# Performance work log

Hardware: AMD Instinct MI355X
Metric: run time of the kernel (lower is better)

Reference implementation:

```python
import jax, jax.numpy as jnp
import numpy as np

N_CHANNELS = 512
N_HEAD = 8
N_GROUPS = 32
EPS = 1e-5


def setup_inputs() -> dict:
    key = jax.random.key(0)
    ks = jax.random.split(key, 12)
    C = N_CHANNELS
    s = 1.0 / np.sqrt(C)
    return {
        "x": jax.random.normal(ks[0], (16, C, 32, 32), dtype=jnp.float32),
        "gn_w": jnp.ones((C,), jnp.float32),
        "gn_b": jnp.zeros((C,), jnp.float32),
        "conv_w": jax.random.normal(ks[1], (C, C), dtype=jnp.float32) * s,  # 1x1 conv kernel [out,in]
        "conv_b": jnp.zeros((C,), jnp.float32),
        "wq": jax.random.normal(ks[2], (C, C), dtype=jnp.float32) * s,  # torch Linear weight [out,in]
        "bq": jnp.zeros((C,), jnp.float32),
        "wk": jax.random.normal(ks[3], (C, C), dtype=jnp.float32) * s,
        "bk": jnp.zeros((C,), jnp.float32),
        "wv": jax.random.normal(ks[4], (C, C), dtype=jnp.float32) * s,
        "bv": jnp.zeros((C,), jnp.float32),
        "wo": jax.random.normal(ks[5], (C, C), dtype=jnp.float32) * s,
        "bo": jnp.zeros((C,), jnp.float32),
    }


def _group_norm(x, w, b):
    # x: [B, C, H, W]; normalize over channel groups + spatial dims
    B, C, H, W = x.shape
    xg = x.reshape(B, N_GROUPS, C // N_GROUPS, H, W)
    mean = jnp.mean(xg, axis=(2, 3, 4), keepdims=True)
    var = jnp.var(xg, axis=(2, 3, 4), keepdims=True)
    xn = ((xg - mean) * jax.lax.rsqrt(var + EPS)).reshape(B, C, H, W)
    return xn * w[None, :, None, None] + b[None, :, None, None]


def reference(x, gn_w, gn_b, conv_w, conv_b, wq, bq, wk, bk, wv, bv, wo, bo):
    B, C, H, W = x.shape
    nh, dk = N_HEAD, C // N_HEAD
    scale = dk ** -0.5

    xn = _group_norm(x, gn_w, gn_b)
    # 1x1 conv == per-pixel linear over channels
    x1 = jnp.einsum("bchw,oc->bohw", xn, conv_w) + conv_b[None, :, None, None]
    # b c h w -> b (h w) c
    x1 = x1.reshape(B, C, H * W).transpose(0, 2, 1)  # [B, L, C]

    q = x1 @ wq.T + bq
    k = x1 @ wk.T + bk
    v = x1 @ wv.T + bv

    L = H * W
    # b l (n d) -> b n l d
    q = q.reshape(B, L, nh, dk).transpose(0, 2, 1, 3)
    k = k.reshape(B, L, nh, dk).transpose(0, 2, 1, 3)
    v = v.reshape(B, L, nh, dk).transpose(0, 2, 1, 3)

    attn = jnp.einsum("bnid,bnjd->bnij", q, k) * scale
    score = jax.nn.softmax(attn, axis=-1)
    res = jnp.einsum("bnij,bnjd->bnid", score, v)

    # b n l d -> b l (n d)
    res = res.transpose(0, 2, 1, 3).reshape(B, L, C)
    res = res @ wo.T + bo
    # b l c -> b c h w
    res = res.transpose(0, 2, 1).reshape(B, C, H, W)
    return res + x
```

## Files before the change

### kernel.cpp

```cpp
#include <hip/hip_runtime.h>
#include <math.h>

typedef __attribute__((ext_vector_type(4))) float f4;
typedef __attribute__((ext_vector_type(16))) float f16v;
typedef __attribute__((ext_vector_type(8))) short s8;
typedef __attribute__((ext_vector_type(4))) unsigned short u16x4;
typedef unsigned short u16;
typedef unsigned int u32;

constexpr int kB = 16, kC = 512, kL = 1024, kNH = 8, kG = 32;
constexpr float kEps = 1e-5f;
constexpr float kQScale = 0.18033688011112042f;

__device__ __forceinline__ u16 f2bf(float f) {
    union { float f; unsigned u; } c; c.f = f;
    unsigned u = c.u;
    return (u16)((u + 0x7fffu + ((u >> 16) & 1u)) >> 16);
}
__device__ __forceinline__ float bf2f(u16 v) {
    union { u32 u; float f; } c; c.u = (u32)v << 16; return c.f;
}
__device__ __forceinline__ u32 pkbf(float lo, float hi) {
    u32 r;
    asm("v_cvt_pk_bf16_f32 %0, %1, %2" : "=v"(r) : "v"(lo), "v"(hi));
    return r;
}

__device__ __forceinline__ void gload_lds16(const void* g, void* l) {
    __builtin_amdgcn_global_load_lds(
        (const __attribute__((address_space(1))) void*)g,
        (__attribute__((address_space(3))) void*)l, 16, 0, 0);
}

__global__ __launch_bounds__(256)
void gn_stats_kernel(const float* __restrict__ x, float2* __restrict__ stats)
{
    const int bg = blockIdx.x;
    const float4* p = (const float4*)(x + (size_t)bg * (16 * kL));
    float s = 0.f, ss = 0.f;
    for (int i = threadIdx.x; i < (16 * kL) / 4; i += 256) {
        float4 v = p[i];
        s  += v.x + v.y + v.z + v.w;
        ss += v.x * v.x + v.y * v.y + v.z * v.z + v.w * v.w;
    }
    #pragma unroll
    for (int off = 32; off > 0; off >>= 1) {
        s  += __shfl_down(s, off);
        ss += __shfl_down(ss, off);
    }
    __shared__ float rs[4], rss[4];
    if ((threadIdx.x & 63) == 0) { rs[threadIdx.x >> 6] = s; rss[threadIdx.x >> 6] = ss; }
    __syncthreads();
    if (threadIdx.x == 0) {
        float S = rs[0] + rs[1] + rs[2] + rs[3];
        float SS = rss[0] + rss[1] + rss[2] + rss[3];
        const float inv_n = 1.f / (float)(16 * kL);
        float mean = S * inv_n;
        float var  = SS * inv_n - mean * mean;
        stats[bg] = make_float2(mean, rsqrtf(var + kEps));
    }
}

__global__ __launch_bounds__(256)
void wprep_kernel(const float* __restrict__ wq, const float* __restrict__ wk,
                  const float* __restrict__ wv, const float* __restrict__ wo,
                  const float* __restrict__ cw,
                  u16* __restrict__ dst, u16* __restrict__ dstT)
{
    __shared__ float t[64][65];
    const int tid = threadIdx.x;
    if (blockIdx.x < 1024) {
        int idx = blockIdx.x * 256 + tid;
        int m = idx >> 16;
        int r = idx & 65535;
        const float* srcs[4] = {wq, wk, wv, wo};
        float4 v = ((const float4*)srcs[m])[r];
        u16x4 o; o.x = f2bf(v.x); o.y = f2bf(v.y); o.z = f2bf(v.z); o.w = f2bf(v.w);
        ((u16x4*)dst)[idx] = o;
    } else {
        int bid = blockIdx.x - 1024;
        const int c0 = (bid >> 3) * 64, e0 = (bid & 7) * 64;
        #pragma unroll
        for (int it = 0; it < 4; ++it) {
            int c = it * 16 + (tid >> 4);
            int e4 = (tid & 15) * 4;
            float4 v = *(const float4*)&cw[(size_t)(c0 + c) * kC + e0 + e4];
            t[c][e4 + 0] = v.x; t[c][e4 + 1] = v.y;
            t[c][e4 + 2] = v.z; t[c][e4 + 3] = v.w;
        }
        __syncthreads();
        #pragma unroll
        for (int it = 0; it < 4; ++it) {
            int e = it * 16 + (tid >> 4);
            int c4 = (tid & 15) * 4;
            u16x4 o;
            o.x = f2bf(t[c4 + 0][e]); o.y = f2bf(t[c4 + 1][e]);
            o.z = f2bf(t[c4 + 2][e]); o.w = f2bf(t[c4 + 3][e]);
            *(u16x4*)&dstT[(size_t)(e0 + e) * kC + c0 + c4] = o;
        }
    }
}

__global__ __launch_bounds__(256)
void bias_fold_kernel(const float* __restrict__ wq, const float* __restrict__ wk,
                      const float* __restrict__ wv, const float* __restrict__ bq,
                      const float* __restrict__ bk, const float* __restrict__ bv,
                      const float* __restrict__ convb, float* __restrict__ outb)
{
    const int o = blockIdx.x * 4 + (threadIdx.x >> 6);
    const int lane = threadIdx.x & 63;
    const float* w; const float* borig; int m2;
    if (o < 512)       { w = wq; borig = bq; m2 = o; }
    else if (o < 1024) { w = wk; borig = bk; m2 = o - 512; }
    else               { w = wv; borig = bv; m2 = o - 1024; }
    const float* wr = w + (size_t)m2 * kC + lane * 8;
    const float* cb = convb + lane * 8;
    float4 a0 = *(const float4*)wr,       a1 = *(const float4*)(wr + 4);
    float4 b0 = *(const float4*)cb,       b1 = *(const float4*)(cb + 4);
    float s = a0.x * b0.x + a0.y * b0.y + a0.z * b0.z + a0.w * b0.w
            + a1.x * b1.x + a1.y * b1.y + a1.z * b1.z + a1.w * b1.w;
    #pragma unroll
    for (int off = 32; off > 0; off >>= 1) s += __shfl_down(s, off);
    if (lane == 0) outb[o] = s + borig[m2];
}

__global__ __launch_bounds__(256)
void gn_t_kernel(const float* __restrict__ x, const float2* __restrict__ stats,
                 const float* __restrict__ gnw, const float* __restrict__ gnb,
                 u16* __restrict__ xt)
{
    __shared__ float t[64][65];
    const int tid = threadIdx.x;
    const int b = blockIdx.z, c0 = blockIdx.y * 64, l0 = blockIdx.x * 64;
    const float* xb = x + ((size_t)(b * kC + c0)) * kL + l0;
    #pragma unroll
    for (int it = 0; it < 4; ++it) {
        int c = it * 16 + (tid >> 4);
        int l4i = (tid & 15) * 4;
        float4 v = *(const float4*)&xb[(size_t)c * kL + l4i];
        float2 st = stats[b * kG + ((c0 + c) >> 4)];
        float a  = st.y * gnw[c0 + c];
        float bb = gnb[c0 + c] - st.x * a;
        t[c][l4i + 0] = v.x * a + bb;
        t[c][l4i + 1] = v.y * a + bb;
        t[c][l4i + 2] = v.z * a + bb;
        t[c][l4i + 3] = v.w * a + bb;
    }
    __syncthreads();
    u16* ob = xt + ((size_t)(b * kL + l0)) * kC + c0;
    #pragma unroll
    for (int it = 0; it < 4; ++it) {
        int l = it * 16 + (tid >> 4);
        int c4 = (tid & 15) * 4;
        u16x4 o;
        o.x = f2bf(t[c4 + 0][l]); o.y = f2bf(t[c4 + 1][l]);
        o.z = f2bf(t[c4 + 2][l]); o.w = f2bf(t[c4 + 3][l]);
        *(u16x4*)&ob[(size_t)l * kC + c4] = o;
    }
}

template <int EPI>
__global__ __launch_bounds__(256)
void gemm_mfma(const u16* __restrict__ W, const u16* __restrict__ X,
               const float* __restrict__ bias0,
               u16* __restrict__ o0, u16* __restrict__ o1, u16* __restrict__ o2,
               const float* __restrict__ resid, float* __restrict__ outf)
{
    __shared__ short lds[2][2][128 * 64];
    const int tid = threadIdx.x, lane = tid & 63, w = tid >> 6;
    const int l15 = lane & 15, l4 = lane >> 4;

    int bxi, byi, bb;
    if constexpr (EPI == 3) {
        bxi = blockIdx.x; byi = blockIdx.y; bb = blockIdx.z;
    } else {
        int f = blockIdx.x;
        int xcd = f & 7, i = f >> 3;
        bb = 2 * xcd + (i & 1);
        int j = i >> 1;
        byi = j >> 3; bxi = j & 7;
    }
    const int bm = byi * 128, bn = bxi * 128;
    const u16* Ag = W + (size_t)bm * kC;
    const u16* Bg = X + ((size_t)bb * kL + bn) * kC;
    const int wm = (w >> 1) * 64, wn = (w & 1) * 64;

    f4 acc[4][4] = {};

    const int srow = w * 32 + (lane >> 3);
    const int sslot = lane & 7;
    size_t ago[4];
    int ldd[4];
    #pragma unroll
    for (int i = 0; i < 4; ++i) {
        int row = srow + i * 8;
        int off = (sslot ^ (row & 7)) << 3;
        ago[i] = (size_t)row * kC + off;
        ldd[i] = (w * 32 + i * 8) * 64;
    }
    auto stage = [&](int kt, int bi) {
        #pragma unroll
        for (int i = 0; i < 4; ++i) {
            gload_lds16(Ag + ago[i] + kt, &lds[bi][0][ldd[i]]);
            gload_lds16(Bg + ago[i] + kt, &lds[bi][1][ldd[i]]);
        }
    };

    int aoff[4][2], boff[4][2];
    #pragma unroll
    for (int f = 0; f < 4; ++f)
        #pragma unroll
        for (int ks = 0; ks < 2; ++ks) {
            int ra = wm + f * 16 + l15;
            aoff[f][ks] = ra * 64 + (((ks * 4 + l4) ^ (ra & 7)) << 3);
            int rb = wn + f * 16 + l15;
            boff[f][ks] = rb * 64 + (((ks * 4 + l4) ^ (rb & 7)) << 3);
        }

    stage(0, 0);

    for (int t = 0; t < 8; ++t) {
        const int cur = t & 1;
        if (t < 7) {
            stage((t + 1) * 64, cur ^ 1);
            asm volatile("s_waitcnt vmcnt(8)" ::: "memory");
        } else {
            asm volatile("s_waitcnt vmcnt(0)" ::: "memory");
        }
        __builtin_amdgcn_s_barrier();

        const short* La = &lds[cur][0][0];
        const short* Lb = &lds[cur][1][0];
        s8 af[4][2], bfr[4][2];
        #pragma unroll
        for (int f = 0; f < 4; ++f)
            #pragma unroll
            for (int ks = 0; ks < 2; ++ks) {
                af[f][ks]  = *(const s8*)(La + aoff[f][ks]);
                bfr[f][ks] = *(const s8*)(Lb + boff[f][ks]);
            }
        #pragma unroll
        for (int fi = 0; fi < 4; ++fi)
            #pragma unroll
            for (int fj = 0; fj < 4; ++fj)
                #pragma unroll
                for (int ks = 0; ks < 2; ++ks)
                    acc[fi][fj] = __builtin_amdgcn_mfma_f32_16x16x32_bf16(
                        af[fi][ks], bfr[fj][ks], acc[fi][fj], 0, 0, 0);

        __builtin_amdgcn_s_barrier();
    }

    #pragma unroll
    for (int fi = 0; fi < 4; ++fi) {
        const int mb = bm + wm + fi * 16 + 4 * l4;
        if constexpr (EPI == 2) {
            #pragma unroll
            for (int fj = 0; fj < 4; ++fj) {
                const int n = bn + wn + fj * 16 + l15;
                #pragma unroll
                for (int r = 0; r < 4; ++r) {
                    size_t idx = ((size_t)(bb * kC + mb + r)) * kL + n;
                    outf[idx] = acc[fi][fj][r] + bias0[mb + r] + resid[idx];
                }
            }
        } else if constexpr (EPI == 3) {
            #pragma unroll
            for (int fj = 0; fj < 4; ++fj) {
                const int n = bn + wn + fj * 16 + l15;
                #pragma unroll
                for (int r = 0; r < 4; ++r)
                    o0[(size_t)(mb + r) * kC + n] = f2bf(acc[fi][fj][r]);
            }
        } else {
            if (mb < 1024) {
                u16* dst = (mb < 512) ? o0 : o1;
                const int m2 = mb & 511;
                float bs[4] = {bias0[mb], bias0[mb + 1], bias0[mb + 2], bias0[mb + 3]};
                #pragma unroll
                for (int fj = 0; fj < 4; ++fj) {
                    const int n = bn + wn + fj * 16 + l15;
                    u16x4 pk;
                    #pragma unroll
                    for (int r = 0; r < 4; ++r) pk[r] = f2bf(acc[fi][fj][r] + bs[r]);
                    *(u16x4*)&dst[((size_t)(bb * kL + n)) * kC + m2] = pk;
                }
            } else {
                const int m2 = mb - 1024;
                #pragma unroll
                for (int fj = 0; fj < 4; ++fj) {
                    const int n = bn + wn + fj * 16 + l15;
                    #pragma unroll
                    for (int r = 0; r < 4; ++r)
                        o2[((size_t)(bb * kC + m2 + r)) * kL + n] =
                            f2bf(acc[fi][fj][r] + bias0[mb + r]);
                }
            }
        }
    }
}

__global__ __launch_bounds__(256, 4)
void attn_mfma(const u16* __restrict__ q, const u16* __restrict__ k,
               const u16* __restrict__ vt, u16* __restrict__ o)
{
    __shared__ short ldsK[2][32 * 128];
    __shared__ short ldsV[2][32 * 128];

    const int tid = threadIdx.x, lane = tid & 63, w = tid >> 6;
    const int l31 = lane & 31, h5 = lane >> 5;

    const int flat = blockIdx.x;
    const int bh = (flat & 7) * 16 + (flat >> 6);
    const int qt = (flat >> 3) & 7;
    const int b = bh >> 3, h = bh & 7;

    const size_t qrow0 = (size_t)b * kL + qt * 128 + w * 32;
    const u16* Qh = q + qrow0 * kC + h * 64;
    const u16* Kb = k + ((size_t)b * kL) * kC + h * 64;
    const u16* Vb = vt + ((size_t)b * kC + h * 64) * kL;

    s8 qf[4];
    #pragma unroll
    for (int ks = 0; ks < 4; ++ks) {
        s8 raw = *(const s8*)(Qh + (size_t)l31 * kC + ks * 16 + h5 * 8);
        #pragma unroll
        for (int e = 0; e < 8; e += 2) {
            u32 pk = pkbf(bf2f((u16)raw[e]) * kQScale,
                          bf2f((u16)raw[e + 1]) * kQScale);
            qf[ks][e]     = (short)(pk & 0xffff);
            qf[ks][e + 1] = (short)(pk >> 16);
        }
    }

    const s8 ones = {0x3F80, 0x3F80, 0x3F80, 0x3F80, 0x3F80, 0x3F80, 0x3F80, 0x3F80};

    f16v oacc0 = {}, oacc1 = {};
    f16v lsum = {};

    size_t kgo[2], vgo[2];
    int ldd[2];
    #pragma unroll
    for (int i = 0; i < 2; ++i) {
        int u_ = w * 128 + i * 64 + lane;
        int row = u_ >> 4, pos = u_ & 15;
        int s = pos ^ (row & 15);
        int jd = row * 2 + (s >> 3);
        int jda = (jd & 51) | ((jd & 4) << 1) | ((jd & 8) >> 1);
        int sub8 = (s & 7) << 3;
        kgo[i] = (size_t)jda * kC + sub8;
        vgo[i] = (size_t)jd * kL + sub8;
        ldd[i] = u_ * 8;
    }
    auto stage = [&](int jt, int bi) {
        #pragma unroll
        for (int i = 0; i < 2; ++i) {
            gload_lds16(Kb + kgo[i] + (size_t)jt * (64 * kC), &ldsK[bi][ldd[i]]);
            gload_lds16(Vb + vgo[i] + jt * 64,                &ldsV[bi][ldd[i]]);
        }
    };

    const int sbase = (l31 & 1) << 3;
    const int rlo = l31 >> 1;
    int loff[4];
    #pragma unroll
    for (int ks = 0; ks < 4; ++ks) {
        int s_ = sbase | (2 * ks + h5);
        loff[ks] = rlo * 128 + ((s_ ^ (rlo & 15)) << 3);
    }

    stage(0, 0);

    for (int t = 0; t < 16; ++t) {
        const int cur = t & 1;
        if (t < 15) {
            stage(t + 1, cur ^ 1);
            asm volatile("s_waitcnt vmcnt(4)" ::: "memory");
        } else {
            asm volatile("s_waitcnt vmcnt(0)" ::: "memory");
        }
        __builtin_amdgcn_s_barrier();

        const short* Kl = ldsK[cur];
        const short* Vl = ldsV[cur];

        f16v sf0 = {}, sf1 = {};
        __builtin_amdgcn_s_setprio(1);
        #pragma unroll
        for (int ks = 0; ks < 4; ++ks) {
            s8 kf0 = *(const s8*)(Kl + loff[ks]);
            s8 kf1 = *(const s8*)(Kl + loff[ks] + 2048);
            sf0 = __builtin_amdgcn_mfma_f32_32x32x16_bf16(kf0, qf[ks], sf0, 0, 0, 0);
            sf1 = __builtin_amdgcn_mfma_f32_32x32x16_bf16(kf1, qf[ks], sf1, 0, 0, 0);
        }
        __builtin_amdgcn_s_setprio(0);

        #pragma unroll
        for (int r = 0; r < 16; ++r) {
            sf0[r] = exp2f(sf0[r]);
            sf1[r] = exp2f(sf1[r]);
        }

        s8 pf[4];
        #pragma unroll
        for (int ks = 0; ks < 4; ++ks) {
            const f16v& pv = (ks < 2) ? sf0 : sf1;
            const int r0 = 8 * (ks & 1);
            union { u32 wd[4]; s8 v; } u;
            u.wd[0] = pkbf(pv[r0 + 0], pv[r0 + 1]);
            u.wd[1] = pkbf(pv[r0 + 2], pv[r0 + 3]);
            u.wd[2] = pkbf(pv[r0 + 4], pv[r0 + 5]);
            u.wd[3] = pkbf(pv[r0 + 6], pv[r0 + 7]);
            pf[ks] = u.v;
        }

        __builtin_amdgcn_s_setprio(1);
        #pragma unroll
        for (int ks = 0; ks < 4; ++ks) {
            lsum = __builtin_amdgcn_mfma_f32_32x32x16_bf16(ones, pf[ks], lsum, 0, 0, 0);
            s8 vf0 = *(const s8*)(Vl + loff[ks]);
            s8 vf1 = *(const s8*)(Vl + loff[ks] + 2048);
            oacc0 = __builtin_amdgcn_mfma_f32_32x32x16_bf16(vf0, pf[ks], oacc0, 0, 0, 0);
            oacc1 = __builtin_amdgcn_mfma_f32_32x32x16_bf16(vf1, pf[ks], oacc1, 0, 0, 0);
        }
        __builtin_amdgcn_s_setprio(0);

        __builtin_amdgcn_s_barrier();
    }

    const float inv = 1.0f / lsum[0];
    u16* orow = o + (qrow0 + l31) * kC + h * 64;
    #pragma unroll
    for (int db = 0; db < 2; ++db) {
        const f16v& oa = db ? oacc1 : oacc0;
        #pragma unroll
        for (int g = 0; g < 4; ++g) {
            int d0 = db * 32 + g * 8 + 4 * h5;
            u32 w0 = pkbf(oa[g * 4 + 0] * inv, oa[g * 4 + 1] * inv);
            u32 w1 = pkbf(oa[g * 4 + 2] * inv, oa[g * 4 + 3] * inv);
            u16x4 pk;
            pk[0] = (u16)(w0 & 0xffff); pk[1] = (u16)(w0 >> 16);
            pk[2] = (u16)(w1 & 0xffff); pk[3] = (u16)(w1 >> 16);
            *(u16x4*)&orow[d0] = pk;
        }
    }
}

extern "C" void kernel_launch(void* const* d_in, const int* in_sizes, int n_in,
                              void* d_out, int out_size, void* d_ws, size_t ws_size,
                              hipStream_t stream)
{
    const float* x      = (const float*)d_in[0];
    const float* gn_w   = (const float*)d_in[1];
    const float* gn_b   = (const float*)d_in[2];
    const float* conv_w = (const float*)d_in[3];
    const float* conv_b = (const float*)d_in[4];
    const float* wq     = (const float*)d_in[5];
    const float* bq     = (const float*)d_in[6];
    const float* wk     = (const float*)d_in[7];
    const float* bk     = (const float*)d_in[8];
    const float* wv     = (const float*)d_in[9];
    const float* bv     = (const float*)d_in[10];
    const float* wo     = (const float*)d_in[11];
    const float* bo     = (const float*)d_in[12];
    float* out = (float*)d_out;

    char* ws = (char*)d_ws;
    float2* stats = (float2*)ws;
    u16* wqkvB  = (u16*)(ws + 8192);
    u16* woB    = wqkvB + 786432;
    u16* convwT = woB + 262144;
    u16* wqkvF  = convwT + 262144;
    float* bqkvF = (float*)(wqkvF + 786432);
    const size_t ACT = (size_t)kB * kL * kC;
    u16* xt  = (u16*)(ws + (6 << 20));
    u16* qb  = xt + ACT;
    u16* kb  = qb + ACT;
    u16* vtb = kb + ACT;
    u16* res = xt;

    wprep_kernel<<<1088, 256, 0, stream>>>(wq, wk, wv, wo, conv_w, wqkvB, convwT);
    gemm_mfma<3><<<dim3(4, 12, 1), 256, 0, stream>>>(
        wqkvB, convwT, nullptr, wqkvF, nullptr, nullptr, nullptr, nullptr);
    bias_fold_kernel<<<384, 256, 0, stream>>>(wq, wk, wv, bq, bk, bv, conv_b, bqkvF);

    gn_stats_kernel<<<kB * kG, 256, 0, stream>>>(x, stats);
    gn_t_kernel<<<dim3(16, 8, kB), 256, 0, stream>>>(x, stats, gn_w, gn_b, xt);

    gemm_mfma<1><<<1536, 256, 0, stream>>>(
        wqkvF, xt, bqkvF, qb, kb, vtb, nullptr, nullptr);
    attn_mfma<<<dim3(1024), 256, 0, stream>>>(qb, kb, vtb, res);
    gemm_mfma<2><<<512, 256, 0, stream>>>(
        woB, res, bo, nullptr, nullptr, nullptr, x, out);
}
```

Measured before the change: 151.7 us.

## Merge prep kernels, halve GEMM K-tile, and enlarge attention blocks to 512 threads

Merges weight conversion, bias folding and group-norm statistics into one prep launch, which removes two kernel launches. The GEMM K-step shrinks from 64 to 32, halving its LDS footprint so more blocks can fit per CU, and adds s_setprio around the MFMA loop. Attention blocks now hold 8 waves covering 256 query rows, so each K/V tile staged in LDS serves twice as many queries. The trade-offs are more barriers per GEMM and lower register budgets under the tighter launch bounds.

Result: slower. 592.1 us (+290.4%).

```diff
diff --git a/kernel.cpp b/kernel.cpp
--- a/kernel.cpp
+++ b/kernel.cpp
@@ -33,53 +33,28 @@
 }
 
 __global__ __launch_bounds__(256)
-void gn_stats_kernel(const float* __restrict__ x, float2* __restrict__ stats)
-{
-    const int bg = blockIdx.x;
-    const float4* p = (const float4*)(x + (size_t)bg * (16 * kL));
-    float s = 0.f, ss = 0.f;
-    for (int i = threadIdx.x; i < (16 * kL) / 4; i += 256) {
-        float4 v = p[i];
-        s  += v.x + v.y + v.z + v.w;
-        ss += v.x * v.x + v.y * v.y + v.z * v.z + v.w * v.w;
-    }
-    #pragma unroll
-    for (int off = 32; off > 0; off >>= 1) {
-        s  += __shfl_down(s, off);
-        ss += __shfl_down(ss, off);
-    }
-    __shared__ float rs[4], rss[4];
-    if ((threadIdx.x & 63) == 0) { rs[threadIdx.x >> 6] = s; rss[threadIdx.x >> 6] = ss; }
-    __syncthreads();
-    if (threadIdx.x == 0) {
-        float S = rs[0] + rs[1] + rs[2] + rs[3];
-        float SS = rss[0] + rss[1] + rss[2] + rss[3];
-        const float inv_n = 1.f / (float)(16 * kL);
-        float mean = S * inv_n;
-        float var  = SS * inv_n - mean * mean;
-        stats[bg] = make_float2(mean, rsqrtf(var + kEps));
-    }
-}
-
-__global__ __launch_bounds__(256)
-void wprep_kernel(const float* __restrict__ wq, const float* __restrict__ wk,
+void prep1_kernel(const float* __restrict__ wq, const float* __restrict__ wk,
                   const float* __restrict__ wv, const float* __restrict__ wo,
-                  const float* __restrict__ cw,
-                  u16* __restrict__ dst, u16* __restrict__ dstT)
+                  const float* __restrict__ cw, const float* __restrict__ bq,
+                  const float* __restrict__ bk, const float* __restrict__ bv,
+                  const float* __restrict__ convb, const float* __restrict__ x,
+                  u16* __restrict__ dst, u16* __restrict__ dstT,
+                  float* __restrict__ outb, float2* __restrict__ stats)
 {
     __shared__ float t[64][65];
     const int tid = threadIdx.x;
-    if (blockIdx.x < 1024) {
-        int idx = blockIdx.x * 256 + tid;
+    const int bid = blockIdx.x;
+    if (bid < 1024) {
+        int idx = bid * 256 + tid;
         int m = idx >> 16;
         int r = idx & 65535;
         const float* srcs[4] = {wq, wk, wv, wo};
         float4 v = ((const float4*)srcs[m])[r];
         u16x4 o; o.x = f2bf(v.x); o.y = f2bf(v.y); o.z = f2bf(v.z); o.w = f2bf(v.w);
         ((u16x4*)dst)[idx] = o;
-    } else {
-        int bid = blockIdx.x - 1024;
-        const int c0 = (bid >> 3) * 64, e0 = (bid & 7) * 64;
+    } else if (bid < 1088) {
+        int b2 = bid - 1024;
+        const int c0 = (b2 >> 3) * 64, e0 = (b2 & 7) * 64;
         #pragma unroll
         for (int it = 0; it < 4; ++it) {
             int c = it * 16 + (tid >> 4);
@@ -98,30 +73,48 @@
             o.z = f2bf(t[c4 + 2][e]); o.w = f2bf(t[c4 + 3][e]);
             *(u16x4*)&dstT[(size_t)(e0 + e) * kC + c0 + c4] = o;
         }
-    }
-}
-
-__global__ __launch_bounds__(256)
-void bias_fold_kernel(const float* __restrict__ wq, const float* __restrict__ wk,
-                      const float* __restrict__ wv, const float* __restrict__ bq,
-                      const float* __restrict__ bk, const float* __restrict__ bv,
-                      const float* __restrict__ convb, float* __restrict__ outb)
-{
-    const int o = blockIdx.x * 4 + (threadIdx.x >> 6);
-    const int lane = threadIdx.x & 63;
-    const float* w; const float* borig; int m2;
-    if (o < 512)       { w = wq; borig = bq; m2 = o; }
-    else if (o < 1024) { w = wk; borig = bk; m2 = o - 512; }
-    else               { w = wv; borig = bv; m2 = o - 1024; }
-    const float* wr = w + (size_t)m2 * kC + lane * 8;
-    const float* cb = convb + lane * 8;
-    float4 a0 = *(const float4*)wr,       a1 = *(const float4*)(wr + 4);
-    float4 b0 = *(const float4*)cb,       b1 = *(const float4*)(cb + 4);
-    float s = a0.x * b0.x + a0.y * b0.y + a0.z * b0.z + a0.w * b0.w
-            + a1.x * b1.x + a1.y * b1.y + a1.z * b1.z + a1.w * b1.w;
-    #pragma unroll
-    for (int off = 32; off > 0; off >>= 1) s += __shfl_down(s, off);
-    if (lane == 0) outb[o] = s + borig[m2];
+    } else if (bid < 1472) {
+        const int o = (bid - 1088) * 4 + (tid >> 6);
+        const int lane = tid & 63;
+        const float* w; const float* borig; int m2;
+        if (o < 512)       { w = wq; borig = bq; m2 = o; }
+        else if (o < 1024) { w = wk; borig = bk; m2 = o - 512; }
+        else               { w = wv; borig = bv; m2 = o - 1024; }
+        const float* wr = w + (size_t)m2 * kC + lane * 8;
+        const float* cb = convb + lane * 8;
+        float4 a0 = *(const float4*)wr,  a1 = *(const float4*)(wr + 4);
+        float4 b0 = *(const float4*)cb,  b1 = *(const float4*)(cb + 4);
+        float s = a0.x * b0.x + a0.y * b0.y + a0.z * b0.z + a0.w * b0.w
+                + a1.x * b1.x + a1.y * b1.y + a1.z * b1.z + a1.w * b1.w;
+        #pragma unroll
+        for (int off = 32; off > 0; off >>= 1) s += __shfl_down(s, off);
+        if (lane == 0) outb[o] = s + borig[m2];
+    } else {
+        const int bg = bid - 1472;
+        const float4* p = (const float4*)(x + (size_t)bg * (16 * kL));
+        float s = 0.f, ss = 0.f;
+        for (int i = tid; i < (16 * kL) / 4; i += 256) {
+            float4 v = p[i];
+            s  += v.x + v.y + v.z + v.w;
+            ss += v.x * v.x + v.y * v.y + v.z * v.z + v.w * v.w;
+        }
+        #pragma unroll
+        for (int off = 32; off > 0; off >>= 1) {
+            s  += __shfl_down(s, off);
+            ss += __shfl_down(ss, off);
+        }
+        __shared__ float rs[4], rss[4];
+        if ((tid & 63) == 0) { rs[tid >> 6] = s; rss[tid >> 6] = ss; }
+        __syncthreads();
+        if (tid == 0) {
+            float S = rs[0] + rs[1] + rs[2] + rs[3];
+            float SS = rss[0] + rss[1] + rss[2] + rss[3];
+            const float inv_n = 1.f / (float)(16 * kL);
+            float mean = S * inv_n;
+            float var  = SS * inv_n - mean * mean;
+            stats[bg] = make_float2(mean, rsqrtf(var + kEps));
+        }
+    }
 }
 
 __global__ __launch_bounds__(256)
@@ -160,13 +153,13 @@
 }
 
 template <int EPI>
-__global__ __launch_bounds__(256)
+__global__ __launch_bounds__(256, 4)
 void gemm_mfma(const u16* __restrict__ W, const u16* __restrict__ X,
                const float* __restrict__ bias0,
                u16* __restrict__ o0, u16* __restrict__ o1, u16* __restrict__ o2,
                const float* __restrict__ resid, float* __restrict__ outf)
 {
-    __shared__ short lds[2][2][128 * 64];
+    __shared__ short lds[2][2][128 * 32];
     const int tid = threadIdx.x, lane = tid & 63, w = tid >> 6;
     const int l15 = lane & 15, l4 = lane >> 4;
 
@@ -187,43 +180,39 @@
 
     f4 acc[4][4] = {};
 
-    const int srow = w * 32 + (lane >> 3);
-    const int sslot = lane & 7;
-    size_t ago[4];
-    int ldd[4];
-    #pragma unroll
-    for (int i = 0; i < 4; ++i) {
-        int row = srow + i * 8;
-        int off = (sslot ^ (row & 7)) << 3;
-        ago[i] = (size_t)row * kC + off;
-        ldd[i] = (w * 32 + i * 8) * 64;
+    size_t ago[2];
+    int ldd[2];
+    #pragma unroll
+    for (int i = 0; i < 2; ++i) {
+        int unit = i * 256 + tid;
+        int row = unit >> 2, pos = unit & 3;
+        ago[i] = (size_t)row * kC + ((pos ^ (row & 3)) << 3);
+        ldd[i] = unit * 8;
     }
     auto stage = [&](int kt, int bi) {
         #pragma unroll
-        for (int i = 0; i < 4; ++i) {
+        for (int i = 0; i < 2; ++i) {
             gload_lds16(Ag + ago[i] + kt, &lds[bi][0][ldd[i]]);
             gload_lds16(Bg + ago[i] + kt, &lds[bi][1][ldd[i]]);
         }
     };
 
-    int aoff[4][2], boff[4][2];
-    #pragma unroll
-    for (int f = 0; f < 4; ++f)
-        #pragma unroll
-        for (int ks = 0; ks < 2; ++ks) {
-            int ra = wm + f * 16 + l15;
-            aoff[f][ks] = ra * 64 + (((ks * 4 + l4) ^ (ra & 7)) << 3);
-            int rb = wn + f * 16 + l15;
-            boff[f][ks] = rb * 64 + (((ks * 4 + l4) ^ (rb & 7)) << 3);
-        }
+    int aoff[4], boff[4];
+    #pragma unroll
+    for (int f = 0; f < 4; ++f) {
+        int ra = wm + f * 16 + l15;
+        aoff[f] = ra * 32 + ((l4 ^ (ra & 3)) << 3);
+        int rb = wn + f * 16 + l15;
+        boff[f] = rb * 32 + ((l4 ^ (rb & 3)) << 3);
+    }
 
     stage(0, 0);
 
-    for (int t = 0; t < 8; ++t) {
+    for (int t = 0; t < 16; ++t) {
         const int cur = t & 1;
-        if (t < 7) {
-            stage((t + 1) * 64, cur ^ 1);
-            asm volatile("s_waitcnt vmcnt(8)" ::: "memory");
+        if (t < 15) {
+            stage((t + 1) * 32, cur ^ 1);
+            asm volatile("s_waitcnt vmcnt(4)" ::: "memory");
         } else {
             asm volatile("s_waitcnt vmcnt(0)" ::: "memory");
         }
@@ -231,22 +220,20 @@
 
         const short* La = &lds[cur][0][0];
         const short* Lb = &lds[cur][1][0];
-        s8 af[4][2], bfr[4][2];
-        #pragma unroll
-        for (int f = 0; f < 4; ++f)
-            #pragma unroll
-            for (int ks = 0; ks < 2; ++ks) {
-                af[f][ks]  = *(const s8*)(La + aoff[f][ks]);
-                bfr[f][ks] = *(const s8*)(Lb + boff[f][ks]);
-            }
+        s8 af[4], bfr[4];
+        #pragma unroll
+        for (int f = 0; f < 4; ++f) {
+            af[f]  = *(const s8*)(La + aoff[f]);
+            bfr[f] = *(const s8*)(Lb + boff[f]);
+        }
+        __builtin_amdgcn_s_setprio(1);
         #pragma unroll
         for (int fi = 0; fi < 4; ++fi)
             #pragma unroll
             for (int fj = 0; fj < 4; ++fj)
-                #pragma unroll
-                for (int ks = 0; ks < 2; ++ks)
-                    acc[fi][fj] = __builtin_amdgcn_mfma_f32_16x16x32_bf16(
-                        af[fi][ks], bfr[fj][ks], acc[fi][fj], 0, 0, 0);
+                acc[fi][fj] = __builtin_amdgcn_mfma_f32_16x16x32_bf16(
+                    af[fi], bfr[fj], acc[fi][fj], 0, 0, 0);
+        __builtin_amdgcn_s_setprio(0);
 
         __builtin_amdgcn_s_barrier();
     }
@@ -300,7 +287,7 @@
     }
 }
 
-__global__ __launch_bounds__(256, 4)
+__global__ __launch_bounds__(512, 8)
 void attn_mfma(const u16* __restrict__ q, const u16* __restrict__ k,
                const u16* __restrict__ vt, u16* __restrict__ o)
 {
@@ -311,11 +298,11 @@
     const int l31 = lane & 31, h5 = lane >> 5;
 
     const int flat = blockIdx.x;
-    const int bh = (flat & 7) * 16 + (flat >> 6);
-    const int qt = (flat >> 3) & 7;
+    const int bh = (flat & 7) * 16 + (flat >> 5);
+    const int qt2 = (flat >> 3) & 3;
     const int b = bh >> 3, h = bh & 7;
 
-    const size_t qrow0 = (size_t)b * kL + qt * 128 + w * 32;
+    const size_t qrow0 = (size_t)b * kL + qt2 * 256 + w * 32;
     const u16* Qh = q + qrow0 * kC + h * 64;
     const u16* Kb = k + ((size_t)b * kL) * kC + h * 64;
     const u16* Vb = vt + ((size_t)b * kC + h * 64) * kL;
@@ -338,26 +325,22 @@
     f16v oacc0 = {}, oacc1 = {};
     f16v lsum = {};
 
-    size_t kgo[2], vgo[2];
-    int ldd[2];
-    #pragma unroll
-    for (int i = 0; i < 2; ++i) {
-        int u_ = w * 128 + i * 64 + lane;
+    size_t kgo, vgo;
+    int ldd;
+    {
+        int u_ = tid;
         int row = u_ >> 4, pos = u_ & 15;
         int s = pos ^ (row & 15);
         int jd = row * 2 + (s >> 3);
         int jda = (jd & 51) | ((jd & 4) << 1) | ((jd & 8) >> 1);
         int sub8 = (s & 7) << 3;
-        kgo[i] = (size_t)jda * kC + sub8;
-        vgo[i] = (size_t)jd * kL + sub8;
-        ldd[i] = u_ * 8;
+        kgo = (size_t)jda * kC + sub8;
+        vgo = (size_t)jd * kL + sub8;
+        ldd = u_ * 8;
     }
     auto stage = [&](int jt, int bi) {
-        #pragma unroll
-        for (int i = 0; i < 2; ++i) {
-            gload_lds16(Kb + kgo[i] + (size_t)jt * (64 * kC), &ldsK[bi][ldd[i]]);
-            gload_lds16(Vb + vgo[i] + jt * 64,                &ldsV[bi][ldd[i]]);
-        }
+        gload_lds16(Kb + kgo + (size_t)jt * (64 * kC), &ldsK[bi][ldd]);
+        gload_lds16(Vb + vgo + jt * 64,                &ldsV[bi][ldd]);
     };
 
     const int sbase = (l31 & 1) << 3;
@@ -375,7 +358,7 @@
         const int cur = t & 1;
         if (t < 15) {
             stage(t + 1, cur ^ 1);
-            asm volatile("s_waitcnt vmcnt(4)" ::: "memory");
+            asm volatile("s_waitcnt vmcnt(2)" ::: "memory");
         } else {
             asm volatile("s_waitcnt vmcnt(0)" ::: "memory");
         }
@@ -479,17 +462,16 @@
     u16* vtb = kb + ACT;
     u16* res = xt;
 
-    wprep_kernel<<<1088, 256, 0, stream>>>(wq, wk, wv, wo, conv_w, wqkvB, convwT);
+    prep1_kernel<<<1984, 256, 0, stream>>>(wq, wk, wv, wo, conv_w,
+                                           bq, bk, bv, conv_b, x,
+                                           wqkvB, convwT, bqkvF, stats);
     gemm_mfma<3><<<dim3(4, 12, 1), 256, 0, stream>>>(
         wqkvB, convwT, nullptr, wqkvF, nullptr, nullptr, nullptr, nullptr);
-    bias_fold_kernel<<<384, 256, 0, stream>>>(wq, wk, wv, bq, bk, bv, conv_b, bqkvF);
-
-    gn_stats_kernel<<<kB * kG, 256, 0, stream>>>(x, stats);
     gn_t_kernel<<<dim3(16, 8, kB), 256, 0, stream>>>(x, stats, gn_w, gn_b, xt);
 
     gemm_mfma<1><<<1536, 256, 0, stream>>>(
         wqkvF, xt, bqkvF, qb, kb, vtb, nullptr, nullptr);
-    attn_mfma<<<dim3(1024), 256, 0, stream>>>(qb, kb, vtb, res);
+    attn_mfma<<<dim3(512), 512, 0, stream>>>(qb, kb, vtb, res);
     gemm_mfma<2><<<512, 256, 0, stream>>>(
         woB, res, bo, nullptr, nullptr, nullptr, x, out);
 }
```
